# Optimization experiments

Measured on AMD Instinct MI355X. Metric: run time of the kernel, lower is better.

## Reference

```python
import jax, jax.numpy as jnp
import numpy as np

STRIDES = (8, 16, 32)
BINS = 16
NC = 80
ALPHA, GAMMA = 0.25, 2.0
W_CLS, W_IOU, W_DFL = 1.0, 7.5, 1.5
B, MAX_GT = 32, 32
EPS = 1e-7


def setup_inputs() -> dict:
    key = jax.random.key(0)
    k0, k1, k2, k3, k4, k5, k6 = jax.random.split(key, 7)
    p0 = jax.random.normal(k0, (B, 4 * BINS + NC, 80, 80), dtype=jnp.float32)
    p1 = jax.random.normal(k1, (B, 4 * BINS + NC, 40, 40), dtype=jnp.float32)
    p2 = jax.random.normal(k2, (B, 4 * BINS + NC, 20, 20), dtype=jnp.float32)
    # realistic xyxy boxes inside a 640x640 image
    c = jax.random.uniform(k3, (B, MAX_GT, 2), minval=60.0, maxval=580.0)
    wh = jax.random.uniform(k4, (B, MAX_GT, 2), minval=16.0, maxval=120.0)
    gt_bboxes = jnp.concatenate([c - wh / 2, c + wh / 2], axis=-1).astype(jnp.float32)
    gt_labels = jax.random.randint(k5, (B, MAX_GT), 0, NC, dtype=jnp.int32)
    raw = jax.random.randint(k6, (B, 8400), 0, 20 * MAX_GT, dtype=jnp.int32)
    matched_gt_inds = jnp.where(raw < MAX_GT, raw, -1)
    return {"p0": p0, "p1": p1, "p2": p2, "gt_bboxes": gt_bboxes,
            "gt_labels": gt_labels, "matched_gt_inds": matched_gt_inds}


def _decode_scale(p, stride):
    # p: [B, 4*BINS + NC, H, W]
    Bp, C, H, W = p.shape
    dfl = p[:, :4 * BINS].reshape(Bp, 4, BINS, H, W)
    cls = p[:, 4 * BINS:]
    # DFL decode: expectation of softmax over bins, scaled by stride
    prob = jax.nn.softmax(dfl, axis=2)
    proj = jnp.arange(BINS, dtype=p.dtype)
    dist = jnp.einsum('bkchw,c->bkhw', prob, proj) * stride  # [B,4,H,W] in pixels
    ys, xs = jnp.meshgrid(jnp.arange(H), jnp.arange(W), indexing='ij')
    cx = ((xs.astype(p.dtype)) + 0.5) * stride
    cy = ((ys.astype(p.dtype)) + 0.5) * stride
    boxes = jnp.stack([cx - dist[:, 0], cy - dist[:, 1],
                       cx + dist[:, 2], cy + dist[:, 3]], axis=-1).reshape(Bp, H * W, 4)
    cls_logits = cls.transpose(0, 2, 3, 1).reshape(Bp, H * W, NC)
    dfl_flat = dfl.transpose(0, 3, 4, 1, 2).reshape(Bp, H * W, 4, BINS)
    grid = jnp.stack([cx, cy], axis=-1).reshape(H * W, 2)
    smap = jnp.full((H * W,), stride, dtype=p.dtype)
    return cls_logits, dfl_flat, boxes, grid, smap


def reference(p0, p1, p2, gt_bboxes, gt_labels, matched_gt_inds):
    outs = [_decode_scale(p, s) for p, s in zip((p0, p1, p2), STRIDES)]
    scores = jnp.concatenate([o[0] for o in outs], axis=1)   # [B,N,NC]
    dfl = jnp.concatenate([o[1] for o in outs], axis=1)      # [B,N,4,BINS]
    pboxes = jnp.concatenate([o[2] for o in outs], axis=1)   # [B,N,4]
    grid = jnp.concatenate([o[3] for o in outs], axis=0)     # [N,2]
    smap = jnp.concatenate([o[4] for o in outs], axis=0)     # [N]

    pos = matched_gt_inds >= 0                               # [B,N]
    idx = jnp.where(pos, matched_gt_inds, 0)
    lbl = jnp.take_along_axis(gt_labels, idx, axis=1)        # [B,N]
    posf = pos.astype(scores.dtype)
    tgt_scores = jax.nn.one_hot(lbl, NC, dtype=scores.dtype) * posf[..., None]

    # sigmoid focal loss (stable BCE-with-logits)
    prob = jax.nn.sigmoid(scores)
    ce = jnp.maximum(scores, 0) - scores * tgt_scores + jnp.log1p(jnp.exp(-jnp.abs(scores)))
    p_t = prob * tgt_scores + (1 - prob) * (1 - tgt_scores)
    alpha_t = tgt_scores * ALPHA + (1 - tgt_scores) * (1 - ALPHA)
    cls_elem = alpha_t * (1.0 - p_t) ** GAMMA * ce
    num_pos = jnp.maximum(posf.sum(), 1.0)
    loss_cls = cls_elem.sum() / num_pos

    # gather matched GT boxes per anchor
    tboxes = jnp.take_along_axis(gt_bboxes, idx[..., None], axis=1)  # [B,N,4]
    gx, gy = grid[None, :, 0], grid[None, :, 1]
    l = jnp.clip(gx - tboxes[..., 0], 0.0)
    t = jnp.clip(gy - tboxes[..., 1], 0.0)
    r = jnp.clip(tboxes[..., 2] - gx, 0.0)
    b_ = jnp.clip(tboxes[..., 3] - gy, 0.0)
    dists = jnp.stack([l, t, r, b_], axis=-1) / smap[None, :, None]   # [B,N,4]
    tb = jnp.clip(dists, 0.0, BINS - 1 - 1e-6)
    lo = jnp.floor(tb).astype(jnp.int32)
    hi = jnp.minimum(lo + 1, BINS - 1)
    a = tb - lo.astype(tb.dtype)
    # soft two-bin DFL target (vectorized form of the scatter_add loop)
    tdist = (jax.nn.one_hot(lo, BINS, dtype=dfl.dtype) * (1.0 - a)[..., None]
             + jax.nn.one_hot(hi, BINS, dtype=dfl.dtype) * a[..., None])   # [B,N,4,BINS]
    logp = jax.nn.log_softmax(dfl, axis=-1)
    dfl_elem = -(tdist * logp).sum(-1)                                # [B,N,4]
    loss_dfl = (dfl_elem * posf[..., None]).sum() / (num_pos * 4.0)

    # IoU loss on positives
    ix1 = jnp.maximum(pboxes[..., 0], tboxes[..., 0])
    iy1 = jnp.maximum(pboxes[..., 1], tboxes[..., 1])
    ix2 = jnp.minimum(pboxes[..., 2], tboxes[..., 2])
    iy2 = jnp.minimum(pboxes[..., 3], tboxes[..., 3])
    inter = jnp.clip(ix2 - ix1, 0.0) * jnp.clip(iy2 - iy1, 0.0)
    area_p = jnp.clip(pboxes[..., 2] - pboxes[..., 0], 0.0) * jnp.clip(pboxes[..., 3] - pboxes[..., 1], 0.0)
    area_t = jnp.clip(tboxes[..., 2] - tboxes[..., 0], 0.0) * jnp.clip(tboxes[..., 3] - tboxes[..., 1], 0.0)
    iou = inter / (area_p + area_t - inter + EPS)
    loss_iou = ((1.0 - iou) * posf).sum() / num_pos

    total = W_CLS * loss_cls + W_IOU * loss_iou + W_DFL * loss_dfl
    return total
```

## Files before the change

### kernel.cpp

```cpp
#include <hip/hip_runtime.h>
#include <math.h>

#define NCLS 80
#define BINS 16
#define BATCH 32
#define MAX_GT 32
#define NA 8400
#define NT 2100
#define NSLOT 64
#define ALPHA_C 0.25f
#define W_CLS 1.0
#define W_IOU 7.5
#define W_DFL 1.5
#define EPS_F 1e-7f

#define IMG_Q4 168000u
#define CLS_Q4 5376000u
#define CLS_GRID 2048
#define CLS_STRIDE (CLS_GRID * 256)

#define POS_GRID 1050
#define NROWS (CLS_GRID + POS_GRID)

__device__ __forceinline__ float focal0(float s)
{
    float e  = __expf(-s);
    float t  = 1.f + e;
    float r  = __builtin_amdgcn_rcpf(t);
    float lg = __logf(t);
    return 0.75f * r * r * (s + lg);
}

__device__ __forceinline__ float focal_corr(float s)
{
    float e  = __expf(-s);
    float t  = 1.f + e;
    float r  = __builtin_amdgcn_rcpf(t);
    float lg = __logf(t);
    return r * r * (0.25f * e * e * lg - 0.75f * (s + lg));
}

__device__ __forceinline__ void block_write4(float c0, float c1, float c2, float c3,
                                             double* __restrict__ row)
{
    #pragma unroll
    for (int o = 32; o > 0; o >>= 1) {
        c0 += __shfl_down(c0, o);
        c1 += __shfl_down(c1, o);
        c2 += __shfl_down(c2, o);
        c3 += __shfl_down(c3, o);
    }
    __shared__ float s4[4][4];
    const int wave = threadIdx.x >> 6, lane = threadIdx.x & 63;
    if (lane == 0) { s4[wave][0] = c0; s4[wave][1] = c1; s4[wave][2] = c2; s4[wave][3] = c3; }
    __syncthreads();
    if (threadIdx.x == 0) {
        row[0] = (double)(s4[0][0] + s4[1][0] + s4[2][0] + s4[3][0]);
        row[1] = (double)(s4[0][1] + s4[1][1] + s4[2][1] + s4[3][1]);
        row[2] = (double)(s4[0][2] + s4[1][2] + s4[2][2] + s4[3][2]);
        row[3] = (double)(s4[0][3] + s4[1][3] + s4[2][3] + s4[3][3]);
    }
}

__device__ __forceinline__ const float4* cls_map(unsigned v,
    const float4* q0, const float4* q1, const float4* q2)
{
    unsigned b  = v / IMG_Q4;
    unsigned r  = v - b * IMG_Q4;
    return (r < 128000u) ? (q0 + (size_t)b * 230400 + 102400 + r)
         : (r < 160000u) ? (q1 + (size_t)b * 57600  + 25600  + (r - 128000u))
                         : (q2 + (size_t)b * 14400  + 6400   + (r - 160000u));
}

__global__ __launch_bounds__(256) void yolo_cls(
    const float* __restrict__ p0, const float* __restrict__ p1, const float* __restrict__ p2,
    double* __restrict__ blk)
{
    const float4* q0 = (const float4*)p0;
    const float4* q1 = (const float4*)p1;
    const float4* q2 = (const float4*)p2;
    const unsigned gtid = blockIdx.x * 256 + threadIdx.x;

    float c = 0.f;
    unsigned vi = gtid;
    #pragma unroll
    for (int rnd = 0; rnd < 2; ++rnd) {
        float4 q[5];
        #pragma unroll
        for (int u = 0; u < 5; ++u)
            q[u] = *cls_map(vi + u * CLS_STRIDE, q0, q1, q2);
        #pragma unroll
        for (int u = 0; u < 5; ++u)
            c += (focal0(q[u].x) + focal0(q[u].y)) + (focal0(q[u].z) + focal0(q[u].w));
        vi += 5 * CLS_STRIDE;
    }
    if (vi < CLS_Q4) {
        float4 q = *cls_map(vi, q0, q1, q2);
        c += (focal0(q.x) + focal0(q.y)) + (focal0(q.z) + focal0(q.w));
    }
    block_write4(c, 0.f, 0.f, 0.f, blk + (size_t)blockIdx.x * 4);
}

template<int HW, int SSTR, int WQ>
__device__ __forceinline__ void pos_scale(
    const float* __restrict__ p, int b, int tl, int k, int gbase, int tid,
    const float* __restrict__ gt_bboxes, const int* __restrict__ gt_labels,
    const int* __restrict__ matched,
    float& c_cls, float& c_iou, float& c_dfl, float& c_cnt)
{
    const int off = tl * 4;
    const int4 m4 = *(const int4*)(matched + (size_t)b * NA + gbase + off);
    const int mm[4] = {m4.x, m4.y, m4.z, m4.w};
    const bool any = (mm[0] >= 0) | (mm[1] >= 0) | (mm[2] >= 0) | (mm[3] >= 0);
    if (!any) return;

    const float stride = (float)SSTR;
    const float inv_s  = 1.f / stride;
    const int h  = tl / WQ;
    const int w0 = (tl - h * WQ) * 4;
    const float cy = ((float)h + 0.5f) * stride;
    const float* pc = p + (size_t)(b * 144 + k * BINS) * HW + off;

    float4 v[BINS];
    #pragma unroll
    for (int i = 0; i < BINS; ++i)
        v[i] = *(const float4*)(pc + (size_t)(i * HW));

    float se[4] = {0.f, 0.f, 0.f, 0.f}, we[4] = {0.f, 0.f, 0.f, 0.f};
    #pragma unroll
    for (int i = 0; i < BINS; ++i) {
        const float wgt = (float)i;
        float e0 = __expf(v[i].x), e1 = __expf(v[i].y);
        float e2 = __expf(v[i].z), e3 = __expf(v[i].w);
        se[0] += e0; we[0] = fmaf(wgt, e0, we[0]);
        se[1] += e1; we[1] = fmaf(wgt, e1, we[1]);
        se[2] += e2; we[2] = fmaf(wgt, e2, we[2]);
        se[3] += e3; we[3] = fmaf(wgt, e3, we[3]);
    }

    float pd[4];
    #pragma unroll
    for (int j = 0; j < 4; ++j) pd[j] = (we[j] / se[j]) * stride;

    #pragma unroll
    for (int j = 0; j < 4; ++j) {
        if (mm[j] >= 0) {
            const float4 tb = *(const float4*)(gt_bboxes + ((size_t)b * MAX_GT + mm[j]) * 4);
            const float cx = ((float)(w0 + j) + 0.5f) * stride;
            float d = (k == 0) ? (cx - tb.x) : (k == 1) ? (cy - tb.y)
                    : (k == 2) ? (tb.z - cx) : (tb.w - cy);
            float tval = fminf(fmaxf(d, 0.f) * inv_s, (float)(BINS - 1) - 1e-6f);
            int   lo = (int)tval;
            float fr = tval - (float)lo;
            float vlo = pc[(size_t)(lo * HW) + j];
            float vhi = pc[(size_t)((lo + 1) * HW) + j];
            float lse = __logf(se[j]);
            c_dfl += -((1.f - fr) * (vlo - lse) + fr * (vhi - lse));
        }
    }

    const int lbase = (tid & 63) & ~3;
    float d1[4], d2[4], d3[4];
    #pragma unroll
    for (int j = 0; j < 4; ++j) {
        d1[j] = __shfl(pd[j], lbase + 1);
        d2[j] = __shfl(pd[j], lbase + 2);
        d3[j] = __shfl(pd[j], lbase + 3);
    }
    if (k == 0) {
        #pragma unroll
        for (int j = 0; j < 4; ++j) {
            if (mm[j] >= 0) {
                const float cx = ((float)(w0 + j) + 0.5f) * stride;
                float px1 = cx - pd[j], py1 = cy - d1[j];
                float px2 = cx + d2[j], py2 = cy + d3[j];
                const float4 tb = *(const float4*)(gt_bboxes + ((size_t)b * MAX_GT + mm[j]) * 4);
                float ix1 = fmaxf(px1, tb.x), iy1 = fmaxf(py1, tb.y);
                float ix2 = fminf(px2, tb.z), iy2 = fminf(py2, tb.w);
                float inter  = fmaxf(ix2 - ix1, 0.f) * fmaxf(iy2 - iy1, 0.f);
                float area_p = fmaxf(px2 - px1, 0.f) * fmaxf(py2 - py1, 0.f);
                float area_t = fmaxf(tb.z - tb.x, 0.f) * fmaxf(tb.w - tb.y, 0.f);
                float iou = inter / (area_p + area_t - inter + EPS_F);
                c_iou += 1.f - iou;
                c_cnt += 1.f;
                int lbl = gt_labels[b * MAX_GT + mm[j]];
                float sv = *(p + (size_t)(b * 144 + 4 * BINS + lbl) * HW + off + j);
                c_cls += focal_corr(sv);
            }
        }
    }
}

__global__ __launch_bounds__(256) void yolo_pos(
    const float* __restrict__ p0, const float* __restrict__ p1, const float* __restrict__ p2,
    const float* __restrict__ gt_bboxes, const int* __restrict__ gt_labels,
    const int* __restrict__ matched, double* __restrict__ blk)
{
    const int tid = (int)threadIdx.x;
    const int gdt = (int)blockIdx.x * 256 + tid;
    const int k   = gdt & 3;
    const int qg  = gdt >> 2;
    const int b   = qg / NT;
    const int t   = qg - b * NT;

    float c_cls = 0.f, c_iou = 0.f, c_dfl = 0.f, c_cnt = 0.f;
    if (t < 1600)
        pos_scale<6400,  8, 20>(p0, b, t,        k, 0,    tid,
                                gt_bboxes, gt_labels, matched, c_cls, c_iou, c_dfl, c_cnt);
    else if (t < 2000)
        pos_scale<1600, 16, 10>(p1, b, t - 1600, k, 6400, tid,
                                gt_bboxes, gt_labels, matched, c_cls, c_iou, c_dfl, c_cnt);
    else
        pos_scale< 400, 32,  5>(p2, b, t - 2000, k, 8000, tid,
                                gt_bboxes, gt_labels, matched, c_cls, c_iou, c_dfl, c_cnt);

    block_write4(c_cls, c_iou, c_dfl, c_cnt, blk + (size_t)(CLS_GRID + blockIdx.x) * 4);
}

__global__ __launch_bounds__(1024) void yolo_finalize_blocks(
    const double* __restrict__ blk, float* __restrict__ out)
{
    const int tid = (int)threadIdx.x;
    double s0 = 0.0, s1 = 0.0, s2 = 0.0, s3 = 0.0;
    for (int r = tid; r < NROWS; r += 1024) {
        const double2* rp = (const double2*)(blk + (size_t)r * 4);
        double2 a = rp[0], b = rp[1];
        s0 += a.x; s1 += a.y; s2 += b.x; s3 += b.y;
    }
    #pragma unroll
    for (int o = 32; o > 0; o >>= 1) {
        s0 += __shfl_down(s0, o); s1 += __shfl_down(s1, o);
        s2 += __shfl_down(s2, o); s3 += __shfl_down(s3, o);
    }
    __shared__ double sh[16][4];
    const int wave = tid >> 6, lane = tid & 63;
    if (lane == 0) { sh[wave][0] = s0; sh[wave][1] = s1; sh[wave][2] = s2; sh[wave][3] = s3; }
    __syncthreads();
    if (tid == 0) {
        double c = 0, i = 0, d = 0, n = 0;
        for (int w = 0; w < 16; ++w) { c += sh[w][0]; i += sh[w][1]; d += sh[w][2]; n += sh[w][3]; }
        double np = (n < 1.0) ? 1.0 : n;
        out[0] = (float)(W_CLS * c / np + W_IOU * i / np + W_DFL * d / (np * 4.0));
    }
}

__device__ __forceinline__ void block_reduce_atomic(float val, double* __restrict__ target)
{
    __shared__ float s[4];
    __syncthreads();
    #pragma unroll
    for (int o = 32; o > 0; o >>= 1) val += __shfl_down(val, o);
    const int wave = threadIdx.x >> 6, lane = threadIdx.x & 63;
    if (lane == 0) s[wave] = val;
    __syncthreads();
    if (threadIdx.x == 0) atomicAdd(target, (double)(s[0] + s[1] + s[2] + s[3]));
}

__device__ __forceinline__ float focal_elem(float s, float tt)
{
    float e   = __expf(-fabsf(s));
    float inv = 1.f / (1.f + e);
    float prob = (s >= 0.f) ? inv : e * inv;
    float ce  = fmaxf(s, 0.f) - s * tt + __logf(1.f + e);
    float p_t = prob * tt + (1.f - prob) * (1.f - tt);
    float alpha_t = tt * ALPHA_C + (1.f - tt) * (1.f - ALPHA_C);
    float om = 1.f - p_t;
    return alpha_t * om * om * ce;
}

__global__ __launch_bounds__(256) void yolo_loss_fused(
    const float* __restrict__ p0, const float* __restrict__ p1, const float* __restrict__ p2,
    const float* __restrict__ gt_bboxes, const int* __restrict__ gt_labels,
    const int* __restrict__ matched, double* __restrict__ acc)
{
    const int a = blockIdx.x * blockDim.x + threadIdx.x;
    const int b = blockIdx.y;
    const int slot = blockIdx.x & (NSLOT - 1);
    float cls_acc = 0.f, iou_acc = 0.f, dfl_acc = 0.f, pos_cnt = 0.f;
    if (a < NA) {
        const float* p; int HW, W; float stride; int off;
        if (a < 6400)      { p = p0; HW = 6400; W = 80; stride = 8.f;  off = a; }
        else if (a < 8000) { p = p1; HW = 1600; W = 40; stride = 16.f; off = a - 6400; }
        else               { p = p2; HW = 400;  W = 20; stride = 32.f; off = a - 8000; }
        const int h = off / W, w = off - h * W;
        const float cx = ((float)w + 0.5f) * stride, cy = ((float)h + 0.5f) * stride;
        const float* pb = p + ((size_t)b * 144) * (size_t)HW + (size_t)off;
        const int m = matched[(size_t)b * NA + a];
        const bool pos = (m >= 0);
        const int idx = pos ? m : 0;
        const int lbl = gt_labels[b * MAX_GT + idx];
        const float* tbp = gt_bboxes + ((size_t)b * MAX_GT + idx) * 4;
        const float tx1 = tbp[0], ty1 = tbp[1], tx2 = tbp[2], ty2 = tbp[3];
        float tdist[4] = {fmaxf(cx - tx1, 0.f) / stride, fmaxf(cy - ty1, 0.f) / stride,
                          fmaxf(tx2 - cx, 0.f) / stride, fmaxf(ty2 - cy, 0.f) / stride};
        float pdv[4]; float dfl_sum = 0.f;
        #pragma unroll
        for (int k = 0; k < 4; ++k) {
            float tv = fminf(tdist[k], (float)(BINS - 1) - 1e-6f);
            int lo = (int)floorf(tv);
            float fr = tv - (float)lo;
            const float* pcx = pb + (size_t)(k * BINS) * HW;
            float v[BINS];
            #pragma unroll
            for (int i = 0; i < BINS; ++i) v[i] = pcx[(size_t)i * HW];
            float mx = v[0];
            #pragma unroll
            for (int i = 1; i < BINS; ++i) mx = fmaxf(mx, v[i]);
            float se = 0.f, we = 0.f, vlo = 0.f, vhi = 0.f;
            #pragma unroll
            for (int i = 0; i < BINS; ++i) {
                float e = __expf(v[i] - mx);
                se += e; we += (float)i * e;
                vlo = (i == lo) ? v[i] : vlo;
                vhi = (i == lo + 1) ? v[i] : vhi;
            }
            pdv[k] = (we / se) * stride;
            if (pos) { float lse = mx + __logf(se); dfl_sum += -((1.f - fr) * (vlo - lse) + fr * (vhi - lse)); }
        }
        const float* pcls = pb + (size_t)(4 * BINS) * HW;
        #pragma unroll 4
        for (int c = 0; c < NCLS; ++c)
            cls_acc += focal_elem(pcls[(size_t)c * HW], (pos && c == lbl) ? 1.f : 0.f);
        if (pos) {
            float px1 = cx - pdv[0], py1 = cy - pdv[1], px2 = cx + pdv[2], py2 = cy + pdv[3];
            float ix1 = fmaxf(px1, tx1), iy1 = fmaxf(py1, ty1);
            float ix2 = fminf(px2, tx2), iy2 = fminf(py2, ty2);
            float inter  = fmaxf(ix2 - ix1, 0.f) * fmaxf(iy2 - iy1, 0.f);
            float area_p = fmaxf(px2 - px1, 0.f) * fmaxf(py2 - py1, 0.f);
            float area_t = fmaxf(tx2 - tx1, 0.f) * fmaxf(ty2 - ty1, 0.f);
            float iou = inter / (area_p + area_t - inter + EPS_F);
            iou_acc = 1.f - iou; dfl_acc = dfl_sum; pos_cnt = 1.f;
        }
    }
    block_reduce_atomic(cls_acc, &acc[0 * NSLOT + slot]);
    block_reduce_atomic(iou_acc, &acc[1 * NSLOT + slot]);
    block_reduce_atomic(dfl_acc, &acc[2 * NSLOT + slot]);
    block_reduce_atomic(pos_cnt, &acc[3 * NSLOT + slot]);
}

__global__ void yolo_loss_finalize(const double* __restrict__ acc, float* __restrict__ out)
{
    double s[4] = {0.0, 0.0, 0.0, 0.0};
    for (int q = 0; q < 4; ++q)
        for (int i = 0; i < NSLOT; ++i) s[q] += acc[q * NSLOT + i];
    double np = s[3] < 1.0 ? 1.0 : s[3];
    double total = W_CLS * s[0] / np + W_IOU * s[1] / np + W_DFL * s[2] / (np * 4.0);
    out[0] = (float)total;
}

extern "C" void kernel_launch(void* const* d_in, const int* in_sizes, int n_in,
                              void* d_out, int out_size, void* d_ws, size_t ws_size,
                              hipStream_t stream)
{
    const float* p0        = (const float*)d_in[0];
    const float* p1        = (const float*)d_in[1];
    const float* p2        = (const float*)d_in[2];
    const float* gt_bboxes = (const float*)d_in[3];
    const int*   gt_labels = (const int*)d_in[4];
    const int*   matched   = (const int*)d_in[5];
    float*  out = (float*)d_out;

    const size_t need = (size_t)NROWS * 4 * sizeof(double);

    if (ws_size >= need) {
        double* blk = (double*)d_ws;
        yolo_cls<<<CLS_GRID, 256, 0, stream>>>(p0, p1, p2, blk);
        yolo_pos<<<POS_GRID, 256, 0, stream>>>(p0, p1, p2, gt_bboxes, gt_labels, matched, blk);
        yolo_finalize_blocks<<<1, 1024, 0, stream>>>(blk, out);
    } else {
        double* acc = (double*)d_ws;
        (void)hipMemsetAsync(acc, 0, 4 * NSLOT * sizeof(double), stream);
        dim3 g((NA + 255) / 256, BATCH);
        yolo_loss_fused<<<g, 256, 0, stream>>>(p0, p1, p2, gt_bboxes, gt_labels, matched, acc);
        yolo_loss_finalize<<<1, 1, 0, stream>>>(acc, out);
    }
}
```

Baseline: 221.8 us.

## Fuse classification and positive-anchor kernels into one 2D-grid kernel

Replaces the separate grid-stride classification focal kernel and the positive-anchor kernel with a single kernel on a (108, batch) grid. Blocks are specialised by x-index: some stream p0 or p1 class logits with fixed per-block chunks, and the rest handle p2 class logits plus the DFL/IoU/positive correction work. Class-logit loads become nontemporal vector loads and the per-element division-based address mapping goes away. This removes one launch and the index arithmetic, at the cost of uneven block workloads and fewer blocks in flight.

New measurement: 210.1 us. 1.06x faster.

```diff
diff --git a/kernel.cpp b/kernel.cpp
--- a/kernel.cpp
+++ b/kernel.cpp
@@ -14,13 +14,13 @@
 #define W_DFL 1.5
 #define EPS_F 1e-7f
 
-#define IMG_Q4 168000u
-#define CLS_Q4 5376000u
-#define CLS_GRID 2048
-#define CLS_STRIDE (CLS_GRID * 256)
-
-#define POS_GRID 1050
-#define NROWS (CLS_GRID + POS_GRID)
+typedef float nf4 __attribute__((ext_vector_type(4)));
+
+#define X_P0 50
+#define X_P1 25
+#define X_POS 33
+#define XDIM (X_P0 + X_P1 + X_POS)
+#define NROWS (XDIM * BATCH)
 
 __device__ __forceinline__ float focal0(float s)
 {
@@ -60,45 +60,6 @@
         row[2] = (double)(s4[0][2] + s4[1][2] + s4[2][2] + s4[3][2]);
         row[3] = (double)(s4[0][3] + s4[1][3] + s4[2][3] + s4[3][3]);
     }
-}
-
-__device__ __forceinline__ const float4* cls_map(unsigned v,
-    const float4* q0, const float4* q1, const float4* q2)
-{
-    unsigned b  = v / IMG_Q4;
-    unsigned r  = v - b * IMG_Q4;
-    return (r < 128000u) ? (q0 + (size_t)b * 230400 + 102400 + r)
-         : (r < 160000u) ? (q1 + (size_t)b * 57600  + 25600  + (r - 128000u))
-                         : (q2 + (size_t)b * 14400  + 6400   + (r - 160000u));
-}
-
-__global__ __launch_bounds__(256) void yolo_cls(
-    const float* __restrict__ p0, const float* __restrict__ p1, const float* __restrict__ p2,
-    double* __restrict__ blk)
-{
-    const float4* q0 = (const float4*)p0;
-    const float4* q1 = (const float4*)p1;
-    const float4* q2 = (const float4*)p2;
-    const unsigned gtid = blockIdx.x * 256 + threadIdx.x;
-
-    float c = 0.f;
-    unsigned vi = gtid;
-    #pragma unroll
-    for (int rnd = 0; rnd < 2; ++rnd) {
-        float4 q[5];
-        #pragma unroll
-        for (int u = 0; u < 5; ++u)
-            q[u] = *cls_map(vi + u * CLS_STRIDE, q0, q1, q2);
-        #pragma unroll
-        for (int u = 0; u < 5; ++u)
-            c += (focal0(q[u].x) + focal0(q[u].y)) + (focal0(q[u].z) + focal0(q[u].w));
-        vi += 5 * CLS_STRIDE;
-    }
-    if (vi < CLS_Q4) {
-        float4 q = *cls_map(vi, q0, q1, q2);
-        c += (focal0(q.x) + focal0(q.y)) + (focal0(q.z) + focal0(q.w));
-    }
-    block_write4(c, 0.f, 0.f, 0.f, blk + (size_t)blockIdx.x * 4);
 }
 
 template<int HW, int SSTR, int WQ>
@@ -191,30 +152,60 @@
     }
 }
 
-__global__ __launch_bounds__(256) void yolo_pos(
+__global__ __launch_bounds__(256) void yolo_main(
     const float* __restrict__ p0, const float* __restrict__ p1, const float* __restrict__ p2,
     const float* __restrict__ gt_bboxes, const int* __restrict__ gt_labels,
     const int* __restrict__ matched, double* __restrict__ blk)
 {
+    const int b   = (int)blockIdx.y;
+    const int x   = (int)blockIdx.x;
     const int tid = (int)threadIdx.x;
-    const int gdt = (int)blockIdx.x * 256 + tid;
-    const int k   = gdt & 3;
-    const int qg  = gdt >> 2;
-    const int b   = qg / NT;
-    const int t   = qg - b * NT;
-
     float c_cls = 0.f, c_iou = 0.f, c_dfl = 0.f, c_cnt = 0.f;
-    if (t < 1600)
-        pos_scale<6400,  8, 20>(p0, b, t,        k, 0,    tid,
-                                gt_bboxes, gt_labels, matched, c_cls, c_iou, c_dfl, c_cnt);
-    else if (t < 2000)
-        pos_scale<1600, 16, 10>(p1, b, t - 1600, k, 6400, tid,
-                                gt_bboxes, gt_labels, matched, c_cls, c_iou, c_dfl, c_cnt);
-    else
-        pos_scale< 400, 32,  5>(p2, b, t - 2000, k, 8000, tid,
-                                gt_bboxes, gt_labels, matched, c_cls, c_iou, c_dfl, c_cnt);
-
-    block_write4(c_cls, c_iou, c_dfl, c_cnt, blk + (size_t)(CLS_GRID + blockIdx.x) * 4);
+
+    if (x < X_P0) {
+        const nf4* q = (const nf4*)p0 + (size_t)b * 230400 + 102400
+                     + (size_t)x * 2560 + tid;
+        nf4 v[10];
+        #pragma unroll
+        for (int i = 0; i < 10; ++i)
+            v[i] = __builtin_nontemporal_load(q + i * 256);
+        #pragma unroll
+        for (int i = 0; i < 10; ++i)
+            c_cls += (focal0(v[i].x) + focal0(v[i].y)) + (focal0(v[i].z) + focal0(v[i].w));
+    } else if (x < X_P0 + X_P1) {
+        const int xx = x - X_P0;
+        const nf4* q = (const nf4*)p1 + (size_t)b * 57600 + 25600
+                     + (size_t)xx * 1280 + tid;
+        nf4 v[5];
+        #pragma unroll
+        for (int i = 0; i < 5; ++i)
+            v[i] = __builtin_nontemporal_load(q + i * 256);
+        #pragma unroll
+        for (int i = 0; i < 5; ++i)
+            c_cls += (focal0(v[i].x) + focal0(v[i].y)) + (focal0(v[i].z) + focal0(v[i].w));
+    } else {
+        const int xx  = x - (X_P0 + X_P1);
+        const int qid = xx * 256 + tid;
+        if (qid < 8000) {
+            nf4 v = __builtin_nontemporal_load(
+                (const nf4*)p2 + (size_t)b * 14400 + 6400 + qid);
+            c_cls += (focal0(v.x) + focal0(v.y)) + (focal0(v.z) + focal0(v.w));
+        }
+        const int t = qid >> 2;
+        const int k = qid & 3;
+        if (t < NT) {
+            if (t < 1600)
+                pos_scale<6400,  8, 20>(p0, b, t,        k, 0,    tid,
+                                        gt_bboxes, gt_labels, matched, c_cls, c_iou, c_dfl, c_cnt);
+            else if (t < 2000)
+                pos_scale<1600, 16, 10>(p1, b, t - 1600, k, 6400, tid,
+                                        gt_bboxes, gt_labels, matched, c_cls, c_iou, c_dfl, c_cnt);
+            else
+                pos_scale< 400, 32,  5>(p2, b, t - 2000, k, 8000, tid,
+                                        gt_bboxes, gt_labels, matched, c_cls, c_iou, c_dfl, c_cnt);
+        }
+    }
+    block_write4(c_cls, c_iou, c_dfl, c_cnt, blk + ((size_t)b * XDIM + x) * 4);
 }
 
 __global__ __launch_bounds__(1024) void yolo_finalize_blocks(
@@ -364,8 +355,8 @@
 
     if (ws_size >= need) {
         double* blk = (double*)d_ws;
-        yolo_cls<<<CLS_GRID, 256, 0, stream>>>(p0, p1, p2, blk);
-        yolo_pos<<<POS_GRID, 256, 0, stream>>>(p0, p1, p2, gt_bboxes, gt_labels, matched, blk);
+        dim3 g(XDIM, BATCH);
+        yolo_main<<<g, 256, 0, stream>>>(p0, p1, p2, gt_bboxes, gt_labels, matched, blk);
         yolo_finalize_blocks<<<1, 1024, 0, stream>>>(blk, out);
     } else {
         double* acc = (double*)d_ws;
```
